# Kernel optimization log

Measured on AMD Instinct MI355X. Metric: run time of the kernel, lower is better.

## Reference

```python
import jax, jax.numpy as jnp
import numpy as np

B, N_IN, N_ALL, NPT, K, C, H = 8, 20000, 1200, 1024, 34, 96, 6
DH = C // H
RADIUS2 = (2.5 * 0.04) ** 2  # grid_size=0.04, sigma=1.0 -> radius 0.1


def _fps(xyz, npoint):
    # furthest point sampling, vectorized over batch, scan over sample steps
    Bb, Nn, _ = xyz.shape
    def step(carry, _):
        dist, far = carry
        cen = jnp.take_along_axis(xyz, far[:, None, None], axis=1)  # [B,1,3]
        d = jnp.sum((xyz - cen) ** 2, -1)                           # [B,N]
        dist = jnp.minimum(dist, d)
        return (dist, jnp.argmax(dist, -1).astype(jnp.int32)), far
    init = (jnp.full((Bb, Nn), 1e10, xyz.dtype), jnp.zeros((Bb,), jnp.int32))
    _, idx = jax.lax.scan(step, init, None, length=npoint)
    return idx.T  # [B, npoint]


def _gather(x, idx):
    return jnp.take_along_axis(x, idx[:, :, None], axis=1)


def _ln(x, g, b):
    m = jnp.mean(x, -1, keepdims=True)
    v = jnp.var(x, -1, keepdims=True)
    return (x - m) * jax.lax.rsqrt(v + 1e-5) * g + b


def _forward(point_clouds, cloud_colors, W_in, b_in, Wq, Wk, Wv, Wo, Wpos, W1, b1, W2, b2, g1, be1, g2, be2, sel):
    fps_idx = _fps(point_clouds, N_ALL)      # [B,1200]
    fps_idx = fps_idx[:, sel]                # random 1024 of 1200 (fixed permutation)
    coord = _gather(point_clouds, fps_idx)   # [B,P,3]
    color = _gather(cloud_colors, fps_idx)   # [B,P,3]
    # ball query within each cloud (all clouds have equal count -> batched dense dists)
    d2 = jnp.sum((coord[:, :, None] - coord[:, None]) ** 2, -1)        # [B,P,P]
    valid = d2 <= RADIUS2
    nidx = jnp.argsort(jnp.where(valid, d2, 1e10), axis=-1)[..., :K]   # [B,P,K]
    nvalid = jnp.take_along_axis(valid, nidx, axis=-1)                 # [B,P,K]
    feat = jnp.concatenate([color, coord], -1)                         # [B,P,6]
    x = feat @ W_in + b_in                                             # [B,P,C]
    q = (x @ Wq).reshape(B, NPT, H, DH)
    k = x @ Wk
    v = x @ Wv
    def gat(t):  # gather per-neighbor features: [B,P,C*] -> [B,P,K,C*]
        return jnp.take_along_axis(t, nidx.reshape(B, NPT * K)[:, :, None], axis=1).reshape(B, NPT, K, -1)
    kn, vn, pn = gat(k), gat(v), gat(coord)
    pe = (coord[:, :, None] - pn) @ Wpos                               # [B,P,K,C] rel-pos enc
    kn = (kn + pe).reshape(B, NPT, K, H, DH)
    vn = (vn + pe).reshape(B, NPT, K, H, DH)
    logits = jnp.einsum('bphd,bpkhd->bphk', q, kn) / jnp.sqrt(jnp.float32(DH))
    logits = jnp.where(nvalid[:, :, None, :], logits, -1e9)
    attn = jax.nn.softmax(logits, -1)
    out = jnp.einsum('bphk,bpkhd->bphd', attn, vn).reshape(B, NPT, C)
    x = _ln(x + out @ Wo, g1, be1)
    x = _ln(x + jax.nn.relu(x @ W1 + b1) @ W2 + b2, g2, be2)
    features = jnp.transpose(x, (0, 2, 1))                             # [B,C,P]
    return features, coord


def setup_inputs() -> dict:
    key = jax.random.key(0)
    ks = jax.random.split(key, 16)
    s = 0.1
    w = lambda k, shp: jax.random.normal(k, shp, jnp.float32) * s
    return {
        'point_clouds': jax.random.uniform(ks[0], (B, N_IN, 3), jnp.float32),
        'cloud_colors': jax.random.uniform(ks[1], (B, N_IN, 3), jnp.float32),
        'W_in': w(ks[2], (6, C)), 'b_in': jnp.zeros((C,), jnp.float32),
        'Wq': w(ks[3], (C, C)), 'Wk': w(ks[4], (C, C)), 'Wv': w(ks[5], (C, C)),
        'Wo': w(ks[6], (C, C)), 'Wpos': w(ks[7], (3, C)),
        'W1': w(ks[8], (C, 4 * C)), 'b1': jnp.zeros((4 * C,), jnp.float32),
        'W2': w(ks[9], (4 * C, C)), 'b2': jnp.zeros((C,), jnp.float32),
        'g1': jnp.ones((C,), jnp.float32), 'be1': jnp.zeros((C,), jnp.float32),
        'g2': jnp.ones((C,), jnp.float32), 'be2': jnp.zeros((C,), jnp.float32),
        'sel': jax.random.permutation(ks[10], N_ALL)[:NPT].astype(jnp.int32),
    }


def reference(point_clouds, cloud_colors, W_in, b_in, Wq, Wk, Wv, Wo, Wpos, W1, b1, W2, b2, g1, be1, g2, be2, sel):
    return _forward(point_clouds, cloud_colors, W_in, b_in, Wq, Wk, Wv, Wo, Wpos, W1, b1, W2, b2, g1, be1, g2, be2, sel)
```

## Files before the change

### kernel.cpp

```cpp
#include <hip/hip_runtime.h>
#include <math.h>

#define B_   8
#define NIN  20000
#define NALL 1200
#define NPTQ 1024
#define KNB  34
#define CH   96
#define FF   384
#define NQ   (B_ * NPTQ)

#define FT   512
#define FPB  8
#define PPB  (NIN / FPB)
#define NPRF 3
#define SPIN_LIM 4096u

typedef unsigned int   u32;
typedef unsigned long long u64;
typedef float v2f __attribute__((ext_vector_type(2)));

__device__ __forceinline__ float scrub(float f) {
    u32 u = __float_as_uint(f);
    return ((u & 0x7F800000u) == 0x7F800000u) ? 12345.0f : f;
}

__global__ __launch_bounds__(FT, 2) void fps_kernel(const float* __restrict__ pc,
                                                    u64* slots,
                                                    int* __restrict__ fps_idx) {
#pragma clang fp contract(off)
    const int blk  = blockIdx.x;
    const int b    = blk >> 3;
    const int part = blk & (FPB - 1);
    const int tid  = threadIdx.x;
    const int lane = tid & 63;
    const int wid  = tid >> 6;
    const float* base = pc + (size_t)b * NIN * 3;
    const int P0 = part * PPB;
    u64* bslot = slots + (size_t)b * NALL * FPB * 4;

    v2f px[NPRF], py[NPRF], pz[NPRF], dist[NPRF];
#pragma unroll
    for (int j = 0; j < NPRF; ++j) {
        int l0 = tid + (2 * j) * FT;
        int l1 = l0 + FT;
        bool ok0 = l0 < PPB;
        bool ok1 = l1 < PPB;
        int a0 = P0 + (ok0 ? l0 : 0);
        int a1 = P0 + (ok1 ? l1 : 0);
        float x0 = base[(size_t)a0 * 3 + 0];
        float y0 = base[(size_t)a0 * 3 + 1];
        float z0 = base[(size_t)a0 * 3 + 2];
        float x1 = base[(size_t)a1 * 3 + 0];
        float y1 = base[(size_t)a1 * 3 + 1];
        float z1 = base[(size_t)a1 * 3 + 2];
        x0 = __shfl(x0, lane); y0 = __shfl(y0, lane); z0 = __shfl(z0, lane);
        x1 = __shfl(x1, lane); y1 = __shfl(y1, lane); z1 = __shfl(z1, lane);
        px[j].x = x0; px[j].y = x1;
        py[j].x = y0; py[j].y = y1;
        pz[j].x = z0; pz[j].y = z1;
        dist[j].x = ok0 ? 1e10f : -1.0f;
        dist[j].y = ok1 ? 1e10f : -1.0f;
    }

    __shared__ u64 rkey[2][8];
    __shared__ u64 win[2][4];

    if (part == 0 && tid == 0) fps_idx[b * NALL + 0] = 0;
    float cx = base[0], cy = base[1], cz = base[2];

    for (int it = 1; it < NALL; ++it) {
        const int pb = it & 1;
        v2f cvx; cvx.x = cx; cvx.y = cx;
        v2f cvy; cvy.x = cy; cvy.y = cy;
        v2f cvz; cvz.x = cz; cvz.y = cz;
        float bd0 = -1e38f, bd1 = -1e38f;
        int bi0 = 0, bi1 = 0;
#pragma unroll
        for (int j = 0; j < NPRF; ++j) {
            v2f dx = px[j] - cvx;
            v2f dy = py[j] - cvy;
            v2f dz = pz[j] - cvz;
            v2f sx = dx * dx;
            v2f sy = dy * dy;
            v2f sz = dz * dz;
            v2f d  = (sx + sy) + sz;
            v2f nd = __builtin_elementwise_min(dist[j], d);
            dist[j] = nd;
            if (nd.x > bd0) { bd0 = nd.x; bi0 = tid + (2 * j) * FT; }
            if (nd.y > bd1) { bd1 = nd.y; bi1 = tid + (2 * j + 1) * FT; }
        }
        u64 k0 = (1ULL << 63) | ((u64)__float_as_uint(bd0) << 16) | (u32)(NIN - (P0 + bi0));
        u64 k1 = (1ULL << 63) | ((u64)__float_as_uint(bd1) << 16) | (u32)(NIN - (P0 + bi1));
        u64 myk = (k1 > k0) ? k1 : k0;
        u64 key = myk;
#pragma unroll
        for (int s = 32; s; s >>= 1) {
            u64 o = __shfl_xor(key, s, 64);
            key = (o > key) ? o : key;
        }
        if (lane == 0) rkey[pb][wid] = key;
        __syncthreads();
        u64 kk = rkey[pb][0];
#pragma unroll
        for (int w = 1; w < 8; ++w) { u64 o = rkey[pb][w]; kk = (o > kk) ? o : kk; }

        if (myk == kk) {
            int lw = (NIN - (int)(kk & 0xFFFFu)) - P0;
            int sl = lw >> 9;
            float wx = 0.f, wy = 0.f, wz = 0.f;
#pragma unroll
            for (int j = 0; j < NPRF; ++j) {
                if (sl == 2 * j)     { wx = px[j].x; wy = py[j].x; wz = pz[j].x; }
                if (sl == 2 * j + 1) { wx = px[j].y; wy = py[j].y; wz = pz[j].y; }
            }
            u64* sp = bslot + (size_t)(it * FPB + part) * 4;
            __hip_atomic_store(sp + 1, (1ULL << 63) | (u64)__float_as_uint(wx),
                               __ATOMIC_RELAXED, __HIP_MEMORY_SCOPE_AGENT);
            __hip_atomic_store(sp + 2, (1ULL << 63) | (u64)__float_as_uint(wy),
                               __ATOMIC_RELAXED, __HIP_MEMORY_SCOPE_AGENT);
            __hip_atomic_store(sp + 3, (1ULL << 63) | (u64)__float_as_uint(wz),
                               __ATOMIC_RELAXED, __HIP_MEMORY_SCOPE_AGENT);
            __hip_atomic_store(sp + 0, kk,
                               __ATOMIC_RELAXED, __HIP_MEMORY_SCOPE_AGENT);
        }

        if (wid == 0) {
            const u64* rowbase = bslot + (size_t)it * FPB * 4;
            u64 w = 0;
            const bool active = lane < 32;
            for (u32 round = 0;; ++round) {
                if (active)
                    w = __hip_atomic_load(rowbase + lane, __ATOMIC_RELAXED,
                                          __HIP_MEMORY_SCOPE_AGENT);
                u64 ball = __ballot((int)(w >> 63));
                if (((ball & 0xFFFFFFFFull) == 0xFFFFFFFFull) || round > SPIN_LIM)
                    break;
            }
            u64 k = __shfl(w, lane & ~3, 64);
            u64 kmax = k;
#pragma unroll
            for (int s = 4; s < 32; s <<= 1) {
                u64 o = __shfl_xor(kmax, s, 64);
                kmax = (o > kmax) ? o : kmax;
            }
            int gw = NIN - (int)(kmax & 0xFFFFu);
            int wpart = gw / PPB;
            u64 xw = __shfl(w, wpart * 4 + 1, 64);
            u64 yw = __shfl(w, wpart * 4 + 2, 64);
            u64 zw = __shfl(w, wpart * 4 + 3, 64);
            if (lane == 0) {
                win[pb][0] = kmax; win[pb][1] = xw;
                win[pb][2] = yw;   win[pb][3] = zw;
            }
        }
        __syncthreads();
        u64 best = win[pb][0];
        int widx = NIN - (int)(best & 0xFFFFu);
        if (part == 0 && tid == 0) fps_idx[b * NALL + it] = widx;
        cx = __uint_as_float((u32)win[pb][1]);
        cy = __uint_as_float((u32)win[pb][2]);
        cz = __uint_as_float((u32)win[pb][3]);
    }
}

__global__ void gather_kernel(const float* __restrict__ pc,
                              const int* __restrict__ fps_idx, const int* __restrict__ sel,
                              float* __restrict__ coord, float* __restrict__ out_coord) {
    int t = blockIdx.x * 256 + threadIdx.x;
    if (t >= NQ) return;
    int b = t >> 10, j = t & 1023;
    int p = fps_idx[b * NALL + sel[j]];
    p = (p < 0) ? 0 : ((p >= NIN) ? (NIN - 1) : p);
    const float* pp = pc + ((size_t)b * NIN + p) * 3;
    float x = pp[0], y = pp[1], z = pp[2];
    coord[(size_t)t * 3 + 0] = x;
    coord[(size_t)t * 3 + 1] = y;
    coord[(size_t)t * 3 + 2] = z;
    out_coord[(size_t)t * 3 + 0] = scrub(x);
    out_coord[(size_t)t * 3 + 1] = scrub(y);
    out_coord[(size_t)t * 3 + 2] = scrub(z);
}

__global__ void knn_kernel(const float* __restrict__ coord, int* __restrict__ nbr) {
    __shared__ float sx[NPTQ], sy[NPTQ], sz[NPTQ];
    const double RAD2D = (2.5 * 0.04) * (2.5 * 0.04);
    int b = blockIdx.x >> 8;
    int i0 = (blockIdx.x & 255) * 4;
    const float* cb = coord + (size_t)b * NPTQ * 3;
    for (int t = threadIdx.x; t < NPTQ; t += 256) {
        sx[t] = cb[(size_t)t * 3 + 0];
        sy[t] = cb[(size_t)t * 3 + 1];
        sz[t] = cb[(size_t)t * 3 + 2];
    }
    __syncthreads();
    int wid = threadIdx.x >> 6, lane = threadIdx.x & 63;
    int i = i0 + wid;
    float qx = sx[i], qy = sy[i], qz = sz[i];
    u64 pk[16];
#pragma unroll
    for (int t = 0; t < 16; ++t) {
        int j = lane + t * 64;
        float dx = __fsub_rn(qx, sx[j]);
        float dy = __fsub_rn(qy, sy[j]);
        float dz = __fsub_rn(qz, sz[j]);
        float d2 = __fadd_rn(__fadd_rn(__fmul_rn(dx, dx), __fmul_rn(dy, dy)),
                             __fmul_rn(dz, dz));
        bool valid = ((double)d2 <= RAD2D);
        pk[t] = valid ? (((u64)__float_as_uint(d2) << 32) | (u32)j) : ~0ull;
    }
    int* out = nbr + ((size_t)b * NPTQ + i) * KNB;
    int k = 0;
    for (; k < KNB; ++k) {
        u64 m = ~0ull;
#pragma unroll
        for (int t = 0; t < 16; ++t) m = (pk[t] < m) ? pk[t] : m;
#pragma unroll
        for (int s = 32; s; s >>= 1) {
            u64 o = __shfl_xor(m, s, 64);
            m = (o < m) ? o : m;
        }
        if (m == ~0ull) break;
#pragma unroll
        for (int t = 0; t < 16; ++t) if (pk[t] == m) pk[t] = ~0ull;
        if (lane == 0) out[k] = (int)(m & 0xFFFFFFFFu);
    }
    for (; k < KNB; ++k) if (lane == 0) out[k] = -1;
}

__global__ void xproj_kernel(const float* __restrict__ pc, const float* __restrict__ col,
                             const int* __restrict__ fps_idx, const int* __restrict__ sel,
                             const float* __restrict__ Win, const float* __restrict__ bin,
                             float* __restrict__ x) {
    int idx = blockIdx.x * 256 + threadIdx.x;
    if (idx >= NQ * CH) return;
    int q = idx / CH, c = idx - q * CH;
    int b = q >> 10, j = q & 1023;
    int p = fps_idx[b * NALL + sel[j]];
    p = (p < 0) ? 0 : ((p >= NIN) ? (NIN - 1) : p);
    const float* pp = pc + ((size_t)b * NIN + p) * 3;
    const float* cc = col + ((size_t)b * NIN + p) * 3;
    float acc = bin[c];
    acc += cc[0] * Win[0 * CH + c];
    acc += cc[1] * Win[1 * CH + c];
    acc += cc[2] * Win[2 * CH + c];
    acc += pp[0] * Win[3 * CH + c];
    acc += pp[1] * Win[4 * CH + c];
    acc += pp[2] * Win[5 * CH + c];
    x[idx] = acc;
}

__global__ void qkv_kernel(const float* __restrict__ x,
                           const float* __restrict__ Wq, const float* __restrict__ Wk,
                           const float* __restrict__ Wv,
                           float* __restrict__ qo, float* __restrict__ ko,
                           float* __restrict__ vo) {
    int idx = blockIdx.x * 256 + threadIdx.x;
    if (idx >= NQ * CH) return;
    int q = idx / CH, c = idx - q * CH;
    const float* xr = x + (size_t)q * CH;
    float aq = 0.f, ak = 0.f, av = 0.f;
    for (int k = 0; k < CH; ++k) {
        float xv = xr[k];
        aq += xv * Wq[k * CH + c];
        ak += xv * Wk[k * CH + c];
        av += xv * Wv[k * CH + c];
    }
    qo[idx] = aq; ko[idx] = ak; vo[idx] = av;
}

__global__ __launch_bounds__(384) void attn_kernel(float* __restrict__ qr1,
                            const float* __restrict__ km, const float* __restrict__ vm,
                            const float* __restrict__ coord, const int* __restrict__ nbr,
                            const float* __restrict__ Wpos, const float* __restrict__ Wo,
                            const float* __restrict__ x) {
    __shared__ float wp[3 * CH];
    __shared__ float os[4][CH];
    for (int t = threadIdx.x; t < 3 * CH; t += 384) wp[t] = Wpos[t];
    __syncthreads();
    int lq = threadIdx.x / CH;
    int c = threadIdx.x - lq * CH;
    int qi = blockIdx.x * 4 + lq;
    int b = qi >> 10, i = qi & 1023;
    const float* crd = coord + (size_t)b * NPTQ * 3;
    float cx = crd[(size_t)i * 3], cy = crd[(size_t)i * 3 + 1], cz = crd[(size_t)i * 3 + 2];
    float qv = qr1[(size_t)qi * CH + c];
    const int* nb = nbr + (size_t)qi * KNB;
    float m = -1e30f, l = 0.f, acc = 0.f;
    for (int t = 0; t < KNB; ++t) {
        int j = nb[t];
        if (j < 0) break;
        float dx = cx - crd[(size_t)j * 3];
        float dy = cy - crd[(size_t)j * 3 + 1];
        float dz = cz - crd[(size_t)j * 3 + 2];
        float pe = dx * wp[c] + dy * wp[CH + c] + dz * wp[2 * CH + c];
        size_t row = (size_t)(b * NPTQ + j) * CH + c;
        float kn = km[row] + pe;
        float s = qv * kn;
        s += __shfl_xor(s, 1); s += __shfl_xor(s, 2);
        s += __shfl_xor(s, 4); s += __shfl_xor(s, 8);
        float logit = s * 0.25f;
        float mn = fmaxf(m, logit);
        float sc = expf(m - mn);
        float p = expf(logit - mn);
        float vn = vm[row] + pe;
        l = l * sc + p;
        acc = acc * sc + p * vn;
        m = mn;
    }
    os[lq][c] = (l > 0.f) ? acc / l : 0.f;
    __syncthreads();
    float r = x[(size_t)qi * CH + c];
    for (int k = 0; k < CH; ++k) r += os[lq][k] * Wo[k * CH + c];
    qr1[(size_t)qi * CH + c] = r;
}

__global__ void ln_kernel(const float* __restrict__ in, const float* __restrict__ g,
                          const float* __restrict__ be, float* __restrict__ out) {
    int row = blockIdx.x * 4 + (threadIdx.x >> 6);
    int lane = threadIdx.x & 63;
    const float* r = in + (size_t)row * CH;
    float e0 = r[lane];
    float e1 = (lane < 32) ? r[64 + lane] : 0.0f;
    float s = e0 + e1;
#pragma unroll
    for (int k = 32; k; k >>= 1) s += __shfl_xor(s, k);
    float mean = s * (1.0f / 96.0f);
    float d0 = e0 - mean, d1 = e1 - mean;
    float vs = d0 * d0 + ((lane < 32) ? d1 * d1 : 0.0f);
#pragma unroll
    for (int k = 32; k; k >>= 1) vs += __shfl_xor(vs, k);
    float rs = 1.0f / sqrtf(vs * (1.0f / 96.0f) + 1e-5f);
    float* o = out + (size_t)row * CH;
    o[lane] = d0 * rs * g[lane] + be[lane];
    if (lane < 32) o[64 + lane] = d1 * rs * g[64 + lane] + be[64 + lane];
}

__global__ __launch_bounds__(384) void ffn_kernel(const float* __restrict__ x2,
                           const float* __restrict__ W1, const float* __restrict__ b1,
                           const float* __restrict__ W2, const float* __restrict__ b2,
                           float* __restrict__ r2) {
    __shared__ float xs[4][CH];
    __shared__ float hs[4][FF];
    __shared__ float ps[4][4][CH];
    int row0 = blockIdx.x * 4, t = threadIdx.x;
    { int r = t / CH, c = t - (t / CH) * CH;
      xs[r][c] = x2[(size_t)(row0 + r) * CH + c]; }
    __syncthreads();
    {
        float bt = b1[t];
        float a0 = bt, a1 = bt, a2 = bt, a3 = bt;
        for (int k = 0; k < CH; ++k) {
            float w = W1[k * FF + t];
            a0 += xs[0][k] * w; a1 += xs[1][k] * w;
            a2 += xs[2][k] * w; a3 += xs[3][k] * w;
        }
        hs[0][t] = fmaxf(a0, 0.f); hs[1][t] = fmaxf(a1, 0.f);
        hs[2][t] = fmaxf(a2, 0.f); hs[3][t] = fmaxf(a3, 0.f);
    }
    __syncthreads();
    {
        int chunk = t / CH, c = t - (t / CH) * CH;
        float p0 = 0.f, p1 = 0.f, p2 = 0.f, p3 = 0.f;
        for (int m = chunk * CH; m < (chunk + 1) * CH; ++m) {
            float w = W2[m * CH + c];
            p0 += hs[0][m] * w; p1 += hs[1][m] * w;
            p2 += hs[2][m] * w; p3 += hs[3][m] * w;
        }
        ps[0][chunk][c] = p0; ps[1][chunk][c] = p1;
        ps[2][chunk][c] = p2; ps[3][chunk][c] = p3;
    }
    __syncthreads();
    { int r = t / CH, c = t - (t / CH) * CH;
      float rr = xs[r][c] + ((ps[r][0][c] + ps[r][1][c]) + (ps[r][2][c] + ps[r][3][c])) + b2[c];
      r2[(size_t)(row0 + r) * CH + c] = rr; }
}

__global__ void ln2t_kernel(const float* __restrict__ in, const float* __restrict__ g,
                            const float* __restrict__ be, float* __restrict__ out) {
    int row = blockIdx.x * 4 + (threadIdx.x >> 6);
    int lane = threadIdx.x & 63;
    int b = row >> 10, i = row & 1023;
    const float* r = in + (size_t)row * CH;
    float e0 = r[lane];
    float e1 = (lane < 32) ? r[64 + lane] : 0.0f;
    float s = e0 + e1;
#pragma unroll
    for (int k = 32; k; k >>= 1) s += __shfl_xor(s, k);
    float mean = s * (1.0f / 96.0f);
    float d0 = e0 - mean, d1 = e1 - mean;
    float vs = d0 * d0 + ((lane < 32) ? d1 * d1 : 0.0f);
#pragma unroll
    for (int k = 32; k; k >>= 1) vs += __shfl_xor(vs, k);
    float rs = 1.0f / sqrtf(vs * (1.0f / 96.0f) + 1e-5f);
    float y0 = d0 * rs * g[lane] + be[lane];
    out[((size_t)(b * CH + lane)) * NPTQ + i] = scrub(y0);
    if (lane < 32) {
        float y1 = d1 * rs * g[64 + lane] + be[64 + lane];
        out[((size_t)(b * CH + 64 + lane)) * NPTQ + i] = scrub(y1);
    }
}

extern "C" void kernel_launch(void* const* d_in, const int* in_sizes, int n_in,
                              void* d_out, int out_size, void* d_ws, size_t ws_size,
                              hipStream_t stream) {
    const float* pc   = (const float*)d_in[0];
    const float* col  = (const float*)d_in[1];
    const float* Win  = (const float*)d_in[2];
    const float* bin  = (const float*)d_in[3];
    const float* Wq   = (const float*)d_in[4];
    const float* Wk   = (const float*)d_in[5];
    const float* Wv   = (const float*)d_in[6];
    const float* Wo   = (const float*)d_in[7];
    const float* Wpos = (const float*)d_in[8];
    const float* W1   = (const float*)d_in[9];
    const float* b1   = (const float*)d_in[10];
    const float* W2   = (const float*)d_in[11];
    const float* b2   = (const float*)d_in[12];
    const float* g1   = (const float*)d_in[13];
    const float* be1  = (const float*)d_in[14];
    const float* g2   = (const float*)d_in[15];
    const float* be2  = (const float*)d_in[16];
    const int*  sel   = (const int*)d_in[17];

    float* out_feat  = (float*)d_out;
    float* out_coord = out_feat + (size_t)B_ * CH * NPTQ;

    char* ws = (char*)d_ws;
    size_t off = 0;
    auto alloc = [&](size_t bytes) { void* p = ws + off; off += (bytes + 255) & ~(size_t)255; return p; };
    int*   w_fps   = (int*)  alloc((size_t)B_ * NALL * 4);
    float* w_coord = (float*)alloc((size_t)NQ * 3 * 4);
    int*   w_nbr   = (int*)  alloc((size_t)NQ * KNB * 4);
    float* w_x     = (float*)alloc((size_t)NQ * CH * 4);
    float* w_q     = (float*)alloc((size_t)NQ * CH * 4);
    float* w_k     = (float*)alloc((size_t)NQ * CH * 4);
    float* w_v     = (float*)alloc((size_t)NQ * CH * 4);
    const size_t slot_bytes = (size_t)B_ * NALL * FPB * 4 * sizeof(u64);
    u64*   w_slots = (u64*)  alloc(slot_bytes);
    (void)ws_size; (void)in_sizes; (void)n_in; (void)out_size;

    hipMemsetAsync(w_slots, 0, slot_bytes, stream);

    fps_kernel<<<B_ * FPB, FT, 0, stream>>>(pc, w_slots, w_fps);

    gather_kernel<<<NQ / 256, 256, 0, stream>>>(pc, w_fps, sel, w_coord, out_coord);
    knn_kernel<<<NQ / 4, 256, 0, stream>>>(w_coord, w_nbr);
    xproj_kernel<<<NQ * CH / 256, 256, 0, stream>>>(pc, col, w_fps, sel, Win, bin, w_x);
    qkv_kernel<<<NQ * CH / 256, 256, 0, stream>>>(w_x, Wq, Wk, Wv, w_q, w_k, w_v);
    attn_kernel<<<NQ / 4, 384, 0, stream>>>(w_q, w_k, w_v, w_coord, w_nbr, Wpos, Wo, w_x);
    ln_kernel<<<NQ / 4, 256, 0, stream>>>(w_q, g1, be1, w_k);
    ffn_kernel<<<NQ / 4, 384, 0, stream>>>(w_k, W1, b1, W2, b2, w_v);
    ln2t_kernel<<<NQ / 4, 256, 0, stream>>>(w_v, g2, be2, out_feat);
}
```

Measured before the change: 3.058 ms.

## Assign FPS batch partitions by XCD and poll slots through a non-coherent fast path

At startup each FPS block records which XCD it runs on, and the 64 blocks are re-ranked so that the 8 partitions of a batch share an XCD where possible. Such co-located groups then poll the cross-block slots with sc0 loads that stay within the XCD's L2 instead of agent-scope atomics. Publishing first writes the slot with two dwordx4 sc0 stores and then repeats the agent-scope stores. The aim is lower latency on the per-iteration inter-block handshake, at the cost of a setup barrier, inline assembly, and reliance on all 64 blocks being co-resident.

Result: slower. 3.202 ms (+4.7%).

```diff
diff --git a/kernel.cpp b/kernel.cpp
--- a/kernel.cpp
+++ b/kernel.cpp
@@ -14,15 +14,40 @@
 #define FPB  8
 #define PPB  (NIN / FPB)
 #define NPRF 3
-#define SPIN_LIM 4096u
+#define SPIN_LIM 8192u
+#define FAST_ROUNDS 32u
+#define SETUP_LIM 4096u
 
 typedef unsigned int   u32;
 typedef unsigned long long u64;
 typedef float v2f __attribute__((ext_vector_type(2)));
+typedef u32 u32x4 __attribute__((ext_vector_type(4)));
 
 __device__ __forceinline__ float scrub(float f) {
     u32 u = __float_as_uint(f);
     return ((u & 0x7F800000u) == 0x7F800000u) ? 12345.0f : f;
+}
+
+__device__ __forceinline__ void slot_publish(u64* sp, u64 kk, u64 xw, u64 yw, u64 zw) {
+    u32x4 lo; lo.x = (u32)kk; lo.y = (u32)(kk >> 32); lo.z = (u32)xw; lo.w = (u32)(xw >> 32);
+    u32x4 hi; hi.x = (u32)yw; hi.y = (u32)(yw >> 32); hi.z = (u32)zw; hi.w = (u32)(zw >> 32);
+    u64 a = (u64)(uintptr_t)sp;
+    asm volatile("global_store_dwordx4 %0, %1, off sc0" :: "v"(a), "v"(lo) : "memory");
+    asm volatile("global_store_dwordx4 %0, %1, off offset:16 sc0" :: "v"(a), "v"(hi) : "memory");
+    __hip_atomic_store(sp + 1, xw, __ATOMIC_RELAXED, __HIP_MEMORY_SCOPE_AGENT);
+    __hip_atomic_store(sp + 2, yw, __ATOMIC_RELAXED, __HIP_MEMORY_SCOPE_AGENT);
+    __hip_atomic_store(sp + 3, zw, __ATOMIC_RELAXED, __HIP_MEMORY_SCOPE_AGENT);
+    __hip_atomic_store(sp + 0, kk, __ATOMIC_RELAXED, __HIP_MEMORY_SCOPE_AGENT);
+}
+
+__device__ __forceinline__ u64 slot_read(const u64* p, bool fast) {
+    if (fast) {
+        u64 w, a = (u64)(uintptr_t)p;
+        asm volatile("global_load_dwordx2 %0, %1, off sc0\n\ts_waitcnt vmcnt(0)"
+                     : "=v"(w) : "v"(a) : "memory");
+        return w;
+    }
+    return __hip_atomic_load(p, __ATOMIC_RELAXED, __HIP_MEMORY_SCOPE_AGENT);
 }
 
 __global__ __launch_bounds__(FT, 2) void fps_kernel(const float* __restrict__ pc,
@@ -30,11 +55,54 @@
                                                     int* __restrict__ fps_idx) {
 #pragma clang fp contract(off)
     const int blk  = blockIdx.x;
-    const int b    = blk >> 3;
-    const int part = blk & (FPB - 1);
     const int tid  = threadIdx.x;
     const int lane = tid & 63;
     const int wid  = tid >> 6;
+
+    __shared__ int s_setup[3];
+    __shared__ u64 rkey[2][8];
+    __shared__ u64 win[2][4];
+
+    {
+        u32 myxcd = ((u32)__builtin_amdgcn_s_getreg((31 << 11) | 20)) & 7u;
+        u64* tbl = slots + (size_t)B_ * NALL * FPB * 4;
+        if (tid == 0)
+            __hip_atomic_store(tbl + blk, (1ULL << 63) | myxcd,
+                               __ATOMIC_RELAXED, __HIP_MEMORY_SCOPE_AGENT);
+        if (tid < 64) {
+            u64 e = 0;
+            for (u32 r = 0;; ++r) {
+                e = __hip_atomic_load(tbl + lane, __ATOMIC_RELAXED,
+                                      __HIP_MEMORY_SCOPE_AGENT);
+                u64 ball = __ballot((int)(e >> 63));
+                if (ball == ~0ull || r > SETUP_LIM) break;
+            }
+            u32 x = (u32)e & 7u;
+            u64 balk[8];
+#pragma unroll
+            for (int k = 0; k < 8; ++k) balk[k] = __ballot(x == (u32)k);
+            u32 Sk = 0;
+#pragma unroll
+            for (int k = 0; k < 8; ++k)
+                if (k < (int)x) Sk += (u32)__popcll(balk[k]);
+            u64 lowmask = (1ull << lane) - 1;
+            u32 rnk = Sk + (u32)__popcll(balk[x] & lowmask);
+            u32 g0 = (rnk >> 3) << 3;
+            int fast_l = (Sk <= g0 && g0 + 8 <= Sk + (u32)__popcll(balk[x])) ? 1 : 0;
+            u32 mine_r = (u32)__shfl((int)rnk, blk, 64);
+            int mine_f = __shfl(fast_l, blk, 64);
+            if (lane == 0) {
+                s_setup[0] = (int)(mine_r >> 3);
+                s_setup[1] = (int)(mine_r & 7u);
+                s_setup[2] = mine_f;
+            }
+        }
+        __syncthreads();
+    }
+    const int b    = s_setup[0];
+    const int part = s_setup[1];
+    bool pollfast  = s_setup[2] != 0;
+
     const float* base = pc + (size_t)b * NIN * 3;
     const int P0 = part * PPB;
     u64* bslot = slots + (size_t)b * NALL * FPB * 4;
@@ -63,9 +131,6 @@
         dist[j].y = ok1 ? 1e10f : -1.0f;
     }
 
-    __shared__ u64 rkey[2][8];
-    __shared__ u64 win[2][4];
-
     if (part == 0 && tid == 0) fps_idx[b * NALL + 0] = 0;
     float cx = base[0], cy = base[1], cz = base[2];
 
@@ -115,28 +180,25 @@
                 if (sl == 2 * j + 1) { wx = px[j].y; wy = py[j].y; wz = pz[j].y; }
             }
             u64* sp = bslot + (size_t)(it * FPB + part) * 4;
-            __hip_atomic_store(sp + 1, (1ULL << 63) | (u64)__float_as_uint(wx),
-                               __ATOMIC_RELAXED, __HIP_MEMORY_SCOPE_AGENT);
-            __hip_atomic_store(sp + 2, (1ULL << 63) | (u64)__float_as_uint(wy),
-                               __ATOMIC_RELAXED, __HIP_MEMORY_SCOPE_AGENT);
-            __hip_atomic_store(sp + 3, (1ULL << 63) | (u64)__float_as_uint(wz),
-                               __ATOMIC_RELAXED, __HIP_MEMORY_SCOPE_AGENT);
-            __hip_atomic_store(sp + 0, kk,
-                               __ATOMIC_RELAXED, __HIP_MEMORY_SCOPE_AGENT);
+            slot_publish(sp, kk,
+                         (1ULL << 63) | (u64)__float_as_uint(wx),
+                         (1ULL << 63) | (u64)__float_as_uint(wy),
+                         (1ULL << 63) | (u64)__float_as_uint(wz));
         }
 
         if (wid == 0) {
             const u64* rowbase = bslot + (size_t)it * FPB * 4;
             u64 w = 0;
             const bool active = lane < 32;
-            for (u32 round = 0;; ++round) {
-                if (active)
-                    w = __hip_atomic_load(rowbase + lane, __ATOMIC_RELAXED,
-                                          __HIP_MEMORY_SCOPE_AGENT);
+            u32 round = 0;
+            for (;; ++round) {
+                bool f = pollfast && round < FAST_ROUNDS;
+                if (active) w = slot_read(rowbase + lane, f);
                 u64 ball = __ballot((int)(w >> 63));
                 if (((ball & 0xFFFFFFFFull) == 0xFFFFFFFFull) || round > SPIN_LIM)
                     break;
             }
+            if (round >= FAST_ROUNDS) pollfast = false;
             u64 k = __shfl(w, lane & ~3, 64);
             u64 kmax = k;
 #pragma unroll
@@ -436,11 +498,11 @@
     float* w_q     = (float*)alloc((size_t)NQ * CH * 4);
     float* w_k     = (float*)alloc((size_t)NQ * CH * 4);
     float* w_v     = (float*)alloc((size_t)NQ * CH * 4);
-    const size_t slot_bytes = (size_t)B_ * NALL * FPB * 4 * sizeof(u64);
+    const size_t slot_bytes = (size_t)B_ * NALL * FPB * 4 * sizeof(u64) + 64 * sizeof(u64);
     u64*   w_slots = (u64*)  alloc(slot_bytes);
     (void)ws_size; (void)in_sizes; (void)n_in; (void)out_size;
 
-    hipMemsetAsync(w_slots, 0, slot_bytes, stream);
+    (void)hipMemsetAsync(w_slots, 0, slot_bytes, stream);
 
     fps_kernel<<<B_ * FPB, FT, 0, stream>>>(pc, w_slots, w_fps);
 
```
